# Performance work log

Measured on AMD Instinct MI355X. Metric: run time of the kernel, lower is better.

## Reference

```python
import jax, jax.numpy as jnp
import numpy as np


def setup_inputs() -> dict:
    key = jax.random.key(0)
    ks = jax.random.split(key, 8)
    C = 256
    Cq = C // 8  # 32
    B, H, W = 4, 64, 64
    x = jax.random.normal(ks[0], (B, C, H, W), dtype=jnp.float32)
    wq = jax.random.normal(ks[1], (Cq, C), dtype=jnp.float32) * (1.0 / np.sqrt(C))
    bq = jax.random.normal(ks[2], (Cq,), dtype=jnp.float32) * 0.01
    wk = jax.random.normal(ks[3], (Cq, C), dtype=jnp.float32) * (1.0 / np.sqrt(C))
    bk = jax.random.normal(ks[4], (Cq,), dtype=jnp.float32) * 0.01
    wv = jax.random.normal(ks[5], (C, C), dtype=jnp.float32) * (1.0 / np.sqrt(C))
    bv = jax.random.normal(ks[6], (C,), dtype=jnp.float32) * 0.01
    gamma = jax.random.normal(ks[7], (1,), dtype=jnp.float32)
    return {"x": x, "wq": wq, "bq": bq, "wk": wk, "bk": bk,
            "wv": wv, "bv": bv, "gamma": gamma}


def reference(x, wq, bq, wk, bk, wv, bv, gamma):
    B, C, H, W = x.shape
    N = H * W
    xf = x.reshape(B, C, N)  # [B, C, N] flattened spatial
    # 1x1 convs == per-position linear projections
    q = jnp.einsum('oc,bcn->bno', wq, xf) + bq          # [B, N, Cq]
    k = jnp.einsum('oc,bcn->bon', wk, xf) + bk[:, None]  # [B, Cq, N]
    v = jnp.einsum('oc,bcn->bon', wv, xf) + bv[:, None]  # [B, C, N]
    attn = jax.nn.softmax(jnp.einsum('bnc,bcm->bnm', q, k), axis=-1)  # [B, N, N]
    # out[b,c,n] = sum_m v[b,c,m] * attn[n,m]
    out = jnp.einsum('bcm,bnm->bcn', v, attn).reshape(B, C, H, W)
    return gamma[0] * out + x
```

## Files before the change

### kernel.cpp

```cpp
#include <hip/hip_runtime.h>

#define BB 4
#define CC 256
#define CQ 32
#define NN 4096

#define QT_OFF 0
#define KT_OFF (BB*NN*CQ)
#define VT_OFF (2*BB*NN*CQ)
#define WB_OFF (VT_OFF + BB*CC*NN)
#define BIAS_OFF (WB_OFF + 320*256)

#define LDS_BARRIER() asm volatile("s_waitcnt lgkmcnt(0)\ns_barrier" ::: "memory")

typedef __attribute__((ext_vector_type(8))) short bf16x8;
typedef __attribute__((ext_vector_type(4))) short bf16x4;
typedef __attribute__((ext_vector_type(4))) float f32x4;

__device__ inline unsigned short f2bf(float f) {
    unsigned int u = __float_as_uint(f);
    u += 0x7fffu + ((u >> 16) & 1u);
    return (unsigned short)(u >> 16);
}

__global__ __launch_bounds__(256) void prepw_kernel(
    const float* __restrict__ wq, const float* __restrict__ bq,
    const float* __restrict__ wk, const float* __restrict__ bk,
    const float* __restrict__ wv, const float* __restrict__ bv,
    unsigned short* __restrict__ ws)
{
    unsigned short* Wb = ws + WB_OFF;
    float* Bias = (float*)(ws + BIAS_OFF);
    int idx = blockIdx.x * 256 + threadIdx.x;
    if (idx < 320 * 256) {
        int row = idx >> 8, col = idx & 255;
        float v = row < 32 ? wq[row * 256 + col]
                : row < 64 ? wk[(row - 32) * 256 + col]
                           : wv[(row - 64) * 256 + col];
        Wb[idx] = f2bf(v);
    }
    if (idx < 320)
        Bias[idx] = idx < 32 ? bq[idx] : idx < 64 ? bk[idx - 32] : bv[idx - 64];
}

__global__ __launch_bounds__(256, 2) void qkv_kernel(
    const float* __restrict__ x, unsigned short* __restrict__ ws)
{
    __shared__ __align__(16) unsigned short xs[32][264];
    __shared__ __align__(16) unsigned short vs[256][40];
    const int t = threadIdx.x;
    const int w = t >> 6, l = t & 63, quad = l >> 4, lc = l & 15;
    const int b = blockIdx.y, n0 = blockIdx.x * 32;

    unsigned short* qT = ws + QT_OFF;
    unsigned short* kT = ws + KT_OFF;
    const unsigned short* Wb = ws + WB_OFF;
    const float* Bias = (const float*)(ws + BIAS_OFF);

    const float* xb = x + (size_t)(b * CC) * NN + n0;
    {
        const int nq = t & 7, swz = (nq & 3) << 3;
#pragma unroll
        for (int p = 0; p < 8; ++p) {
            int c = p * 32 + (t >> 3);
            float4 v4 = *(const float4*)&xb[(size_t)c * NN + nq * 4];
            int cs = c ^ swz;
            xs[nq * 4 + 0][cs] = f2bf(v4.x);
            xs[nq * 4 + 1][cs] = f2bf(v4.y);
            xs[nq * 4 + 2][cs] = f2bf(v4.z);
            xs[nq * 4 + 3][cs] = f2bf(v4.w);
        }
    }
    __syncthreads();

    f32x4 acc[5][2];
#pragma unroll
    for (int j = 0; j < 5; ++j) {
        f32x4 b4 = *(const f32x4*)&Bias[(w * 5 + j) * 16 + quad * 4];
        acc[j][0] = b4; acc[j][1] = b4;
    }

#pragma unroll
    for (int s = 0; s < 8; ++s) {
        bf16x8 Af[5], Bf[2];
#pragma unroll
        for (int j = 0; j < 5; ++j)
            Af[j] = *(const bf16x8*)&Wb[((w * 5 + j) * 16 + lc) * 256 + s * 32 + quad * 8];
#pragma unroll
        for (int nt = 0; nt < 2; ++nt) {
            int pos = nt * 16 + lc;
            int col = (s * 32 + quad * 8) ^ (((pos >> 2) & 3) << 3);
            Bf[nt] = *(const bf16x8*)&xs[pos][col];
        }
#pragma unroll
        for (int j = 0; j < 5; ++j)
#pragma unroll
            for (int nt = 0; nt < 2; ++nt)
                acc[j][nt] = __builtin_amdgcn_mfma_f32_16x16x32_bf16(Af[j], Bf[nt], acc[j][nt], 0, 0, 0);
    }

#pragma unroll
    for (int j = 0; j < 5; ++j) {
        int ot = w * 5 + j;
#pragma unroll
        for (int nt = 0; nt < 2; ++nt) {
            if (ot < 4) {
                bf16x4 pk;
#pragma unroll
                for (int i = 0; i < 4; ++i) pk[i] = (short)f2bf(acc[j][nt][i]);
                unsigned short* bas = (ot < 2 ? qT : kT);
                int ocl = (ot & 1) * 16 + quad * 4;
                *(bf16x4*)&bas[((size_t)(b * NN + n0 + nt * 16 + lc)) * CQ + ocl] = pk;
            } else {
#pragma unroll
                for (int i = 0; i < 4; ++i)
                    vs[(ot - 4) * 16 + quad * 4 + i][nt * 16 + lc] = f2bf(acc[j][nt][i]);
            }
        }
    }
    __syncthreads();

    const int mt = n0 >> 6, hb = (n0 >> 5) & 1;
    unsigned short* vt = ws + VT_OFF + ((size_t)(b * 64 + mt) * 16) * 1024 + hb * 512;
#pragma unroll
    for (int p = 0; p < 4; ++p) {
        int ci = p * 256 + t;
        int ct = ci >> 6, g = (ci >> 4) & 3, lcp = ci & 15;
        bf16x8 chunk = *(const bf16x8*)&vs[ct * 16 + lcp][g * 8];
        *(bf16x8*)&vt[(size_t)ct * 1024 + g * 128 + lcp * 8] = chunk;
    }
}

__global__ __launch_bounds__(512, 2) void attn_kernel(
    const float* __restrict__ x, const unsigned short* __restrict__ ws,
    const float* __restrict__ gamma, float* __restrict__ out)
{
    __shared__ __align__(16) unsigned short Ps[2][4][4][512];
    __shared__ __align__(16) float lSpart[2][64];

    const int t = threadIdx.x;
    const int w = t >> 6, l = t & 63, quad = l >> 4, lc = l & 15;
    const int id = blockIdx.x, xcd = id & 7;
    const int b = xcd >> 1;
    const int n0 = (((id >> 3) << 1) | (xcd & 1)) * 64;

    const int qg = w & 3;
    const int kh = w >> 2;
    const int cb = w * 32;

    const unsigned short* qT = ws + QT_OFF;
    const unsigned short* kb = ws + KT_OFF + (size_t)b * NN * CQ;
    const unsigned short* vb = ws + VT_OFF + ((size_t)b << 20);

    const bf16x8 bqf =
        *(const bf16x8*)&qT[((size_t)(b * NN + n0 + qg * 16 + lc)) * CQ + quad * 8];

    bf16x8 kA[4], kB[4];
    auto loadK = [&](bf16x8* kr, int tt) {
        int m0 = (tt & 31) * 128 + kh * 64;
#pragma unroll
        for (int j = 0; j < 4; ++j)
            kr[j] = *(const bf16x8*)&kb[(size_t)(m0 + j * 16 + lc) * CQ + quad * 8];
    };

    bf16x8 vA[2][4], vB[2][4];
    auto loadV = [&](bf16x8 (*vr)[4], int tt) {
#pragma unroll
        for (int c = 0; c < 2; ++c) {
            int ct = w * 2 + c;
#pragma unroll
            for (int k4 = 0; k4 < 4; ++k4) {
                int m = (tt & 31) * 2 + (k4 >> 1);
                vr[c][k4] = *(const bf16x8*)&vb[((size_t)m * 16 + ct) * 1024 + (k4 & 1) * 512 + l * 8];
            }
        }
    };

    f32x4 acc[4][2];
#pragma unroll
    for (int i = 0; i < 4; ++i)
#pragma unroll
        for (int j = 0; j < 2; ++j) acc[i][j] = (f32x4){0.f, 0.f, 0.f, 0.f};
    f32x4 sn[4];
    float lacc = 0.f;
    const f32x4 z = {0.f, 0.f, 0.f, 0.f};

    auto expstore = [&](int pp) {
#pragma unroll
        for (int j = 0; j < 4; ++j) {
            bf16x4 pk;
#pragma unroll
            for (int i = 0; i < 4; ++i) {
                float p = __expf(sn[j][i]);
                lacc += p;
                pk[i] = (short)f2bf(p);
            }
            int ks = kh * 2 + (j >> 1);
            int lanep = ((2 * j + (quad >> 1)) & 3) * 16 + lc;
            *(bf16x4*)&Ps[pp][qg][ks][lanep * 8 + (quad & 1) * 4] = pk;
        }
    };

    auto pv = [&](int pp, bf16x8 (*vr)[4]) {
#pragma unroll
        for (int ks = 0; ks < 4; ++ks)
#pragma unroll
            for (int qs = 0; qs < 4; ++qs) {
                bf16x8 ap = *(const bf16x8*)&Ps[pp][qs][ks][l * 8];
#pragma unroll
                for (int c = 0; c < 2; ++c)
                    acc[qs][c] = __builtin_amdgcn_mfma_f32_16x16x32_bf16(ap, vr[c][ks], acc[qs][c], 0, 0, 0);
            }
    };

    auto body = [&](int tt, int pp, bf16x8* kUse, bf16x8* kNext,
                    bf16x8 (*vUse)[4], bf16x8 (*vNext)[4]) {
        loadV(vNext, tt + 1);
#pragma unroll
        for (int j = 0; j < 4; ++j)
            sn[j] = __builtin_amdgcn_mfma_f32_16x16x32_bf16(kUse[j], bqf, z, 0, 0, 0);
        loadK(kNext, tt + 2);
        expstore(pp ^ 1);
        pv(pp, vUse);
        LDS_BARRIER();
    };

    loadK(kA, 0);
#pragma unroll
    for (int j = 0; j < 4; ++j)
        sn[j] = __builtin_amdgcn_mfma_f32_16x16x32_bf16(kA[j], bqf, z, 0, 0, 0);
    loadK(kA, 1);
    expstore(0);
    loadV(vA, 0);
    LDS_BARRIER();

    for (int it = 0; it < 15; ++it) {
        body(2 * it,     0, kA, kB, vA, vB);
        body(2 * it + 1, 1, kB, kA, vB, vA);
    }
    body(30, 0, kA, kB, vA, vB);
    pv(1, vB);

    lacc += __shfl_xor(lacc, 16);
    lacc += __shfl_xor(lacc, 32);
    if (quad == 0) lSpart[kh][qg * 16 + lc] = lacc;
    LDS_BARRIER();

    const float g = gamma[0];
#pragma unroll
    for (int qs = 0; qs < 4; ++qs) {
        f32x4 l0 = *(const f32x4*)&lSpart[0][qs * 16 + quad * 4];
        f32x4 l1 = *(const f32x4*)&lSpart[1][qs * 16 + quad * 4];
        f32x4 rl;
#pragma unroll
        for (int i = 0; i < 4; ++i) rl[i] = 1.f / (l0[i] + l1[i]);
#pragma unroll
        for (int c2 = 0; c2 < 2; ++c2) {
            int c = cb + c2 * 16 + lc;
            size_t base = ((size_t)(b * CC + c)) * NN + n0 + qs * 16 + quad * 4;
            f32x4 xr = *(const f32x4*)&x[base];
            f32x4 o;
#pragma unroll
            for (int i = 0; i < 4; ++i) o[i] = g * acc[qs][c2][i] * rl[i] + xr[i];
            *(f32x4*)&out[base] = o;
        }
    }
}

extern "C" void kernel_launch(void* const* d_in, const int* in_sizes, int n_in,
                              void* d_out, int out_size, void* d_ws, size_t ws_size,
                              hipStream_t stream) {
    const float* x     = (const float*)d_in[0];
    const float* wq    = (const float*)d_in[1];
    const float* bq    = (const float*)d_in[2];
    const float* wk    = (const float*)d_in[3];
    const float* bk    = (const float*)d_in[4];
    const float* wv    = (const float*)d_in[5];
    const float* bv    = (const float*)d_in[6];
    const float* gamma = (const float*)d_in[7];
    float* out = (float*)d_out;
    unsigned short* ws = (unsigned short*)d_ws;

    prepw_kernel<<<320, 256, 0, stream>>>(wq, bq, wk, bk, wv, bv, ws);
    dim3 g1(NN / 32, BB);
    qkv_kernel<<<g1, 256, 0, stream>>>(x, ws);
    attn_kernel<<<256, 512, 0, stream>>>(x, ws, gamma, out);
}
```

Measured before the change: 144.9 us.

## Interleave softmax exp with PV MFMAs and vectorize x-to-bf16 LDS stores

The attention loop now processes one k-slice at a time. It loads the P fragments, computes and stores one exp chunk, then issues that slice's PV MFMAs with raised wave priority, so exp/VALU work overlaps with matrix work. The QKV staging loads four channel rows per thread and writes packed bf16x4 to LDS instead of scalar shorts, reducing LDS store count. Register pressure may rise, and the changed access pattern may alter bank conflicts.

After: 145.0 us. No clear change (+0.1%).

```diff
diff --git a/kernel.cpp b/kernel.cpp
--- a/kernel.cpp
+++ b/kernel.cpp
@@ -61,14 +61,22 @@
     {
         const int nq = t & 7, swz = (nq & 3) << 3;
 #pragma unroll
-        for (int p = 0; p < 8; ++p) {
-            int c = p * 32 + (t >> 3);
-            float4 v4 = *(const float4*)&xb[(size_t)c * NN + nq * 4];
-            int cs = c ^ swz;
-            xs[nq * 4 + 0][cs] = f2bf(v4.x);
-            xs[nq * 4 + 1][cs] = f2bf(v4.y);
-            xs[nq * 4 + 2][cs] = f2bf(v4.z);
-            xs[nq * 4 + 3][cs] = f2bf(v4.w);
+        for (int u = 0; u < 2; ++u) {
+            const int c0 = (t >> 3) * 4 + u * 128;
+            f32x4 r0 = *(const f32x4*)&xb[(size_t)(c0 + 0) * NN + nq * 4];
+            f32x4 r1 = *(const f32x4*)&xb[(size_t)(c0 + 1) * NN + nq * 4];
+            f32x4 r2 = *(const f32x4*)&xb[(size_t)(c0 + 2) * NN + nq * 4];
+            f32x4 r3 = *(const f32x4*)&xb[(size_t)(c0 + 3) * NN + nq * 4];
+            const int cs = c0 ^ swz;
+#pragma unroll
+            for (int k = 0; k < 4; ++k) {
+                bf16x4 w4;
+                w4[0] = (short)f2bf(r0[k]);
+                w4[1] = (short)f2bf(r1[k]);
+                w4[2] = (short)f2bf(r2[k]);
+                w4[3] = (short)f2bf(r3[k]);
+                *(bf16x4*)&xs[nq * 4 + k][cs] = w4;
+            }
         }
     }
     __syncthreads();
@@ -185,32 +193,27 @@
     float lacc = 0.f;
     const f32x4 z = {0.f, 0.f, 0.f, 0.f};
 
-    auto expstore = [&](int pp) {
-#pragma unroll
-        for (int j = 0; j < 4; ++j) {
-            bf16x4 pk;
-#pragma unroll
-            for (int i = 0; i < 4; ++i) {
-                float p = __expf(sn[j][i]);
-                lacc += p;
-                pk[i] = (short)f2bf(p);
-            }
-            int ks = kh * 2 + (j >> 1);
-            int lanep = ((2 * j + (quad >> 1)) & 3) * 16 + lc;
-            *(bf16x4*)&Ps[pp][qg][ks][lanep * 8 + (quad & 1) * 4] = pk;
-        }
-    };
-
-    auto pv = [&](int pp, bf16x8 (*vr)[4]) {
-#pragma unroll
-        for (int ks = 0; ks < 4; ++ks)
-#pragma unroll
-            for (int qs = 0; qs < 4; ++qs) {
-                bf16x8 ap = *(const bf16x8*)&Ps[pp][qs][ks][l * 8];
-#pragma unroll
-                for (int c = 0; c < 2; ++c)
-                    acc[qs][c] = __builtin_amdgcn_mfma_f32_16x16x32_bf16(ap, vr[c][ks], acc[qs][c], 0, 0, 0);
-            }
+    auto expj = [&](int pp, int j) {
+        bf16x4 pk;
+#pragma unroll
+        for (int i = 0; i < 4; ++i) {
+            float p = __expf(sn[j][i]);
+            lacc += p;
+            pk[i] = (short)f2bf(p);
+        }
+        int ks = kh * 2 + (j >> 1);
+        int lanep = ((2 * j + (quad >> 1)) & 3) * 16 + lc;
+        *(bf16x4*)&Ps[pp][qg][ks][lanep * 8 + (quad & 1) * 4] = pk;
+    };
+
+    auto pvks = [&](int ks, bf16x8 (*vr)[4], const bf16x8* ap) {
+        __builtin_amdgcn_s_setprio(1);
+#pragma unroll
+        for (int qs = 0; qs < 4; ++qs)
+#pragma unroll
+            for (int c = 0; c < 2; ++c)
+                acc[qs][c] = __builtin_amdgcn_mfma_f32_16x16x32_bf16(ap[qs], vr[c][ks], acc[qs][c], 0, 0, 0);
+        __builtin_amdgcn_s_setprio(0);
     };
 
     auto body = [&](int tt, int pp, bf16x8* kUse, bf16x8* kNext,
@@ -220,8 +223,15 @@
         for (int j = 0; j < 4; ++j)
             sn[j] = __builtin_amdgcn_mfma_f32_16x16x32_bf16(kUse[j], bqf, z, 0, 0, 0);
         loadK(kNext, tt + 2);
-        expstore(pp ^ 1);
-        pv(pp, vUse);
+#pragma unroll
+        for (int ks = 0; ks < 4; ++ks) {
+            bf16x8 ap[4];
+#pragma unroll
+            for (int qs = 0; qs < 4; ++qs)
+                ap[qs] = *(const bf16x8*)&Ps[pp][qs][ks][l * 8];
+            expj(pp ^ 1, ks);
+            pvks(ks, vUse, ap);
+        }
         LDS_BARRIER();
     };
 
@@ -230,7 +240,8 @@
     for (int j = 0; j < 4; ++j)
         sn[j] = __builtin_amdgcn_mfma_f32_16x16x32_bf16(kA[j], bqf, z, 0, 0, 0);
     loadK(kA, 1);
-    expstore(0);
+#pragma unroll
+    for (int j = 0; j < 4; ++j) expj(0, j);
     loadV(vA, 0);
     LDS_BARRIER();
 
@@ -239,7 +250,14 @@
         body(2 * it + 1, 1, kB, kA, vB, vA);
     }
     body(30, 0, kA, kB, vA, vB);
-    pv(1, vB);
+#pragma unroll
+    for (int ks = 0; ks < 4; ++ks) {
+        bf16x8 ap[4];
+#pragma unroll
+        for (int qs = 0; qs < 4; ++qs)
+            ap[qs] = *(const bf16x8*)&Ps[1][qs][ks][l * 8];
+        pvks(ks, vB, ap);
+    }
 
     lacc += __shfl_xor(lacc, 16);
     lacc += __shfl_xor(lacc, 32);
```
